# Kernel tuning notes

Hardware: AMD Instinct MI355X
Metric: run time of the kernel (lower is better)

## Reference

```python
import jax, jax.numpy as jnp
import numpy as np

B, CTX = 16, 64
H, W = 1024, 1024
EPS = 1e-12
STD = 0.001


def setup_inputs() -> dict:
    key = jax.random.key(0)
    ks = jax.random.split(key, 6)
    x = jax.random.normal(ks[0], (B, CTX), dtype=jnp.float32)
    # context_transform_input / gate: Linear(CTX -> 12) with bias
    lim = 1.0 / np.sqrt(CTX)
    W_in = jax.random.uniform(ks[1], (12, CTX), jnp.float32, -lim, lim)
    b_in = jax.random.uniform(ks[2], (12,), jnp.float32, -lim, lim)
    W_gate = jax.random.uniform(ks[3], (12, CTX), jnp.float32, -lim, lim)
    b_gate = jax.random.uniform(ks[4], (12,), jnp.float32, -lim, lim)
    # base weights: [1, 2, 2, H, W, 2], normal(0, STD)
    weights = STD * jax.random.normal(ks[5], (1, 2, 2, H, W, 2), dtype=jnp.float32)
    return {"x": x, "W_in": W_in, "b_in": b_in, "W_gate": W_gate,
            "b_gate": b_gate, "weights": weights}


def _clerp(z1, z2, c):
    # complex lerp: z1 + c*(z2 - z1) with complex c packed in last dim
    c0, c1 = c[..., 0], c[..., 1]
    re = (1 - c0) * z1[..., 0] + c0 * z2[..., 0] - c1 * (z2[..., 1] - z1[..., 1])
    im = (1 - c0) * z1[..., 1] + c0 * z2[..., 1] + c1 * (z2[..., 0] - z1[..., 0])
    return jnp.stack([re, im], axis=-1)


def _caddmul(z1, z2, bias):
    # bias + z1*z2 (complex), packed in last dim
    re = bias[..., 0] + (z1[..., 0] * z2[..., 0] - z1[..., 1] * z2[..., 1])
    im = bias[..., 1] + (z1[..., 0] * z2[..., 1] + z1[..., 1] * z2[..., 0])
    return jnp.stack([re, im], axis=-1)


def reference(x, W_in, b_in, W_gate, b_gate, weights):
    b = x.shape[0]
    x_t = x @ W_in.T + b_in          # [B, 12]
    x_g = x @ W_gate.T + b_gate      # [B, 12]
    mod = (x_t * jnp.tanh(x_g)).reshape(b, 3, 2, 1, 1, 2)  # broadcasts over H, W
    shift_lerp = jnp.array([0.5, 0.0], dtype=x.dtype)
    shift_scale = jnp.array([1.0, 0.0], dtype=x.dtype)
    param_l = mod[:, 0] + shift_lerp   # [B, 2, 1, 1, 2]
    param_b = mod[:, 1]
    param_s = mod[:, 2] + shift_scale
    w0, w1 = weights[:, 0], weights[:, 1]   # [1, 2, H, W, 2] each
    z = _clerp(w0, w1, param_l)             # [B, 2, H, W, 2]
    z = _caddmul(z, param_s, param_b)       # [B, 2, H, W, 2]
    denom = jnp.sqrt(jnp.sum(z[:, 1] ** 2, axis=-1) + EPS)[..., None]  # [B, H, W, 1]
    theta = z[:, 1] / denom
    return jnp.sum(z[:, 0] * theta, axis=-1)  # [B, H, W]
```

## Files before the change

kernel.cpp:

```cpp
#include <hip/hip_runtime.h>
#include <math.h>

#define HW (1024*1024)
#define BATCH 16

typedef float fx4 __attribute__((ext_vector_type(4)));

__global__ __launch_bounds__(256) void fused_kernel(
    const float* __restrict__ x,
    const float* __restrict__ W_in,
    const float* __restrict__ b_in,
    const float* __restrict__ W_gate,
    const float* __restrict__ b_gate,
    const float* __restrict__ wts,
    float* __restrict__ out)
{
    __shared__ float smod[BATCH][12];
    __shared__ float sp[192];
    int t = threadIdx.x;

    if (t < 192) {
        int b = t / 12, j = t % 12;
        const float4* x4  = (const float4*)(x + b * 64);
        const float4* wi4 = (const float4*)(W_in + j * 64);
        const float4* wg4 = (const float4*)(W_gate + j * 64);
        float xt = b_in[j], xg = b_gate[j];
#pragma unroll
        for (int k = 0; k < 16; ++k) {
            float4 xv = x4[k], wi = wi4[k], wg = wg4[k];
            xt = fmaf(xv.x, wi.x, xt); xg = fmaf(xv.x, wg.x, xg);
            xt = fmaf(xv.y, wi.y, xt); xg = fmaf(xv.y, wg.y, xg);
            xt = fmaf(xv.z, wi.z, xt); xg = fmaf(xv.z, wg.z, xg);
            xt = fmaf(xv.w, wi.w, xt); xg = fmaf(xv.w, wg.w, xg);
        }
        smod[b][j] = xt * tanhf(xg);
    }
    __syncthreads();
    if (t < 32) {
        int bb = t >> 1, c = t & 1;
        float l0 = smod[bb][0 * 4 + c * 2 + 0] + 0.5f;
        float l1 = smod[bb][0 * 4 + c * 2 + 1];
        float br = smod[bb][1 * 4 + c * 2 + 0];
        float bi = smod[bb][1 * 4 + c * 2 + 1];
        float s0 = smod[bb][2 * 4 + c * 2 + 0] + 1.0f;
        float s1 = smod[bb][2 * 4 + c * 2 + 1];
        float omr = 1.0f - l0, omi = -l1;
        float Ar = s0 * omr - s1 * omi;
        float Ai = s0 * omi + s1 * omr;
        float Br = s0 * l0 - s1 * l1;
        float Bi = s0 * l1 + s1 * l0;
        float* p = sp + (bb * 2 + c) * 6;
        p[0] = Ar; p[1] = Ai; p[2] = Br; p[3] = Bi; p[4] = br; p[5] = bi;
    }
    __syncthreads();

    int idx = blockIdx.x * 256 + t;
    const float4* w4 = (const float4*)wts;

    float4 Wv[4][2];
#pragma unroll
    for (int jc = 0; jc < 4; ++jc) {
        Wv[jc][0] = w4[jc * (HW / 2) + idx * 2 + 0];
        Wv[jc][1] = w4[jc * (HW / 2) + idx * 2 + 1];
    }
    const float* w00 = (const float*)Wv[0];
    const float* w01 = (const float*)Wv[1];
    const float* w10 = (const float*)Wv[2];
    const float* w11 = (const float*)Wv[3];

    fx4* out4 = (fx4*)out;
#pragma unroll
    for (int b = 0; b < BATCH; ++b) {
        const float* p0 = &sp[(b * 2 + 0) * 6];
        const float* p1 = &sp[(b * 2 + 1) * 6];
        float A0r = p0[0], A0i = p0[1], B0r = p0[2], B0i = p0[3], c0r = p0[4], c0i = p0[5];
        float A1r = p1[0], A1i = p1[1], B1r = p1[2], B1i = p1[3], c1r = p1[4], c1i = p1[5];
        fx4 o;
#pragma unroll
        for (int p = 0; p < 4; ++p) {
            float a0r = w00[p * 2], a0i = w00[p * 2 + 1];
            float b0r = w10[p * 2], b0i = w10[p * 2 + 1];
            float a1r = w01[p * 2], a1i = w01[p * 2 + 1];
            float b1r = w11[p * 2], b1i = w11[p * 2 + 1];
            float z0r = c0r + A0r * a0r - A0i * a0i + B0r * b0r - B0i * b0i;
            float z0i = c0i + A0r * a0i + A0i * a0r + B0r * b0i + B0i * b0r;
            float z1r = c1r + A1r * a1r - A1i * a1i + B1r * b1r - B1i * b1i;
            float z1i = c1i + A1r * a1i + A1i * a1r + B1r * b1i + B1i * b1r;
            float rs = rsqrtf(z1r * z1r + z1i * z1i + 1e-12f);
            o[p] = (z0r * z1r + z0i * z1i) * rs;
        }
        __builtin_nontemporal_store(o, &out4[b * (HW / 4) + idx]);
    }
}

extern "C" void kernel_launch(void* const* d_in, const int* in_sizes, int n_in,
                              void* d_out, int out_size, void* d_ws, size_t ws_size,
                              hipStream_t stream) {
    const float* x      = (const float*)d_in[0];
    const float* W_in   = (const float*)d_in[1];
    const float* b_in   = (const float*)d_in[2];
    const float* W_gate = (const float*)d_in[3];
    const float* b_gate = (const float*)d_in[4];
    const float* wts    = (const float*)d_in[5];
    float* out = (float*)d_out;

    fused_kernel<<<1024, 256, 0, stream>>>(x, W_in, b_in, W_gate, b_gate, wts, out);
}
```

Measured before the change: 32.73 us.

## Specialize an extra wavefront for the modulation prologue, overlapping the weight loads

The block grows from 256 to 320 threads. The first 256 threads issue their weight loads before the barrier, while a dedicated extra wavefront computes the 12 gated projections per batch and the per-batch complex coefficients. This removes one __syncthreads and hides the prologue latency behind the global loads. The coefficient reads from shared memory are vectorized into three 16-byte loads, and the nontemporal output store becomes a regular store. Risks: the extra wavefront idles after the barrier and can reduce occupancy. The in-wavefront shared-memory handoff with no barrier relies on a 64-wide wavefront.

```diff
diff --git a/kernel.cpp b/kernel.cpp
--- a/kernel.cpp
+++ b/kernel.cpp
@@ -6,7 +6,7 @@
 
 typedef float fx4 __attribute__((ext_vector_type(4)));
 
-__global__ __launch_bounds__(256) void fused_kernel(
+__global__ __launch_bounds__(320, 5) void fused_kernel(
     const float* __restrict__ x,
     const float* __restrict__ W_in,
     const float* __restrict__ b_in,
@@ -17,65 +17,76 @@
 {
     __shared__ float smod[BATCH][12];
     __shared__ float sp[192];
-    int t = threadIdx.x;
+    const int t = threadIdx.x;
 
-    if (t < 192) {
-        int b = t / 12, j = t % 12;
-        const float4* x4  = (const float4*)(x + b * 64);
-        const float4* wi4 = (const float4*)(W_in + j * 64);
-        const float4* wg4 = (const float4*)(W_gate + j * 64);
-        float xt = b_in[j], xg = b_gate[j];
+    float4 Wv[4][2];
+    int idx = 0;
+    if (t < 256) {
+        idx = blockIdx.x * 256 + t;
+        const float4* w4 = (const float4*)wts;
 #pragma unroll
-        for (int k = 0; k < 16; ++k) {
-            float4 xv = x4[k], wi = wi4[k], wg = wg4[k];
-            xt = fmaf(xv.x, wi.x, xt); xg = fmaf(xv.x, wg.x, xg);
-            xt = fmaf(xv.y, wi.y, xt); xg = fmaf(xv.y, wg.y, xg);
-            xt = fmaf(xv.z, wi.z, xt); xg = fmaf(xv.z, wg.z, xg);
-            xt = fmaf(xv.w, wi.w, xt); xg = fmaf(xv.w, wg.w, xg);
+        for (int jc = 0; jc < 4; ++jc) {
+            Wv[jc][0] = w4[jc * (HW / 2) + idx * 2 + 0];
+            Wv[jc][1] = w4[jc * (HW / 2) + idx * 2 + 1];
         }
-        smod[b][j] = xt * tanhf(xg);
+    } else {
+        const int u = t - 256;
+#pragma unroll
+        for (int r = 0; r < 3; ++r) {
+            int id = u * 3 + r;
+            int b = id / 12, j = id % 12;
+            const float4* x4  = (const float4*)(x + b * 64);
+            const float4* wi4 = (const float4*)(W_in + j * 64);
+            const float4* wg4 = (const float4*)(W_gate + j * 64);
+            float xt = b_in[j], xg = b_gate[j];
+#pragma unroll
+            for (int k = 0; k < 16; ++k) {
+                float4 xv = x4[k], wi = wi4[k], wg = wg4[k];
+                xt = fmaf(xv.x, wi.x, xt); xg = fmaf(xv.x, wg.x, xg);
+                xt = fmaf(xv.y, wi.y, xt); xg = fmaf(xv.y, wg.y, xg);
+                xt = fmaf(xv.z, wi.z, xt); xg = fmaf(xv.z, wg.z, xg);
+                xt = fmaf(xv.w, wi.w, xt); xg = fmaf(xv.w, wg.w, xg);
+            }
+            smod[b][j] = xt * tanhf(xg);
+        }
+        if (u < 32) {
+            int bb = u >> 1, c = u & 1;
+            float l0 = smod[bb][0 + c * 2 + 0] + 0.5f;
+            float l1 = smod[bb][0 + c * 2 + 1];
+            float br = smod[bb][4 + c * 2 + 0];
+            float bi = smod[bb][4 + c * 2 + 1];
+            float s0 = smod[bb][8 + c * 2 + 0] + 1.0f;
+            float s1 = smod[bb][8 + c * 2 + 1];
+            float omr = 1.0f - l0, omi = -l1;
+            float Ar = s0 * omr - s1 * omi;
+            float Ai = s0 * omi + s1 * omr;
+            float Br = s0 * l0 - s1 * l1;
+            float Bi = s0 * l1 + s1 * l0;
+            float* p = sp + u * 6;
+            p[0] = Ar; p[1] = Ai; p[2] = Br; p[3] = Bi; p[4] = br; p[5] = bi;
+        }
     }
     __syncthreads();
-    if (t < 32) {
-        int bb = t >> 1, c = t & 1;
-        float l0 = smod[bb][0 * 4 + c * 2 + 0] + 0.5f;
-        float l1 = smod[bb][0 * 4 + c * 2 + 1];
-        float br = smod[bb][1 * 4 + c * 2 + 0];
-        float bi = smod[bb][1 * 4 + c * 2 + 1];
-        float s0 = smod[bb][2 * 4 + c * 2 + 0] + 1.0f;
-        float s1 = smod[bb][2 * 4 + c * 2 + 1];
-        float omr = 1.0f - l0, omi = -l1;
-        float Ar = s0 * omr - s1 * omi;
-        float Ai = s0 * omi + s1 * omr;
-        float Br = s0 * l0 - s1 * l1;
-        float Bi = s0 * l1 + s1 * l0;
-        float* p = sp + (bb * 2 + c) * 6;
-        p[0] = Ar; p[1] = Ai; p[2] = Br; p[3] = Bi; p[4] = br; p[5] = bi;
-    }
-    __syncthreads();
+    if (t >= 256) return;
 
-    int idx = blockIdx.x * 256 + t;
-    const float4* w4 = (const float4*)wts;
-
-    float4 Wv[4][2];
-#pragma unroll
-    for (int jc = 0; jc < 4; ++jc) {
-        Wv[jc][0] = w4[jc * (HW / 2) + idx * 2 + 0];
-        Wv[jc][1] = w4[jc * (HW / 2) + idx * 2 + 1];
-    }
     const float* w00 = (const float*)Wv[0];
     const float* w01 = (const float*)Wv[1];
     const float* w10 = (const float*)Wv[2];
     const float* w11 = (const float*)Wv[3];
 
-    fx4* out4 = (fx4*)out;
+    float4* out4 = (float4*)out;
 #pragma unroll
     for (int b = 0; b < BATCH; ++b) {
-        const float* p0 = &sp[(b * 2 + 0) * 6];
-        const float* p1 = &sp[(b * 2 + 1) * 6];
-        float A0r = p0[0], A0i = p0[1], B0r = p0[2], B0i = p0[3], c0r = p0[4], c0i = p0[5];
-        float A1r = p1[0], A1i = p1[1], B1r = p1[2], B1i = p1[3], c1r = p1[4], c1i = p1[5];
-        fx4 o;
+        const fx4* q = (const fx4*)(sp + b * 12);
+        fx4 q0 = q[0];
+        fx4 q1 = q[1];
+        fx4 q2 = q[2];
+        float A0r = q0[0], A0i = q0[1], B0r = q0[2], B0i = q0[3];
+        float c0r = q1[0], c0i = q1[1], A1r = q1[2], A1i = q1[3];
+        float B1r = q2[0], B1i = q2[1], c1r = q2[2], c1i = q2[3];
+
+        float4 o;
+        float* op = (float*)&o;
 #pragma unroll
         for (int p = 0; p < 4; ++p) {
             float a0r = w00[p * 2], a0i = w00[p * 2 + 1];
@@ -87,9 +98,9 @@
             float z1r = c1r + A1r * a1r - A1i * a1i + B1r * b1r - B1i * b1i;
             float z1i = c1i + A1r * a1i + A1i * a1r + B1r * b1i + B1i * b1r;
             float rs = rsqrtf(z1r * z1r + z1i * z1i + 1e-12f);
-            o[p] = (z0r * z1r + z0i * z1i) * rs;
+            op[p] = (z0r * z1r + z0i * z1i) * rs;
         }
-        __builtin_nontemporal_store(o, &out4[b * (HW / 4) + idx]);
+        out4[b * (HW / 4) + idx] = o;
     }
 }
 
@@ -104,5 +115,5 @@
     const float* wts    = (const float*)d_in[5];
     float* out = (float*)d_out;
 
-    fused_kernel<<<1024, 256, 0, stream>>>(x, W_in, b_in, W_gate, b_gate, wts, out);
+    fused_kernel<<<1024, 320, 0, stream>>>(x, W_in, b_in, W_gate, b_gate, wts, out);
 }
```

Result: slower. 49.66 us (+51.7%).
